# Optimization experiments

Measured on AMD Instinct MI355X. Metric: run time of the kernel, lower is better.

The kernel has to match this reference:

```python
import jax, jax.numpy as jnp
from jax import lax
import numpy as np

# ---- dims / neuron params (match init_kwargs) ----
B, T, ENC, HID = 256, 500, 700, 128
TAU_MEM = 20.0      # tauSr == tauRef == tau_mem
THETA = 1.0         # spike_threshold
SCALE_REF = 1.0
WIDTH_GRAD = 1.0    # tauRho (surrogate width)
SCALE_GRAD = 1.0    # scaleRho (surrogate scale)


def alpha_filter(x, tau, mult):
    """Causal convolution along axis 0 with SLAYER's alpha (SRM) kernel
    h[k] = mult * (k/tau) * exp(1 - k/tau), Ts = 1.  Implemented as an exact
    2-state linear recurrence instead of an O(T^2) FIR conv.
    x: (T, ...) -> y: (T, ...)
    """
    d = jnp.exp(-1.0 / tau)          # per-step decay
    c = mult * jnp.exp(1.0) / tau    # h[k] = c * k * d**k

    def step(carry, xt):
        p, q = carry
        qn = d * q + c * d * p       # output at t (h[0] = 0)
        pn = d * p + xt
        return (pn, qn), qn

    z = jnp.zeros_like(x[0])
    _, y = lax.scan(step, (z, z), x)
    return y


def _spike_core(u):
    """SLAYER getSpikes: at each t, membrane = psp + accumulated refractory
    response (alpha kernel with mult = -2*theta*scaleRef, tau = tauRef) of all
    past spikes; emit spike (1/Ts) when membrane >= theta.
    u: (T, B, C) psp values -> (spikes, post-refractory membrane), both (T, B, C).
    """
    d = jnp.exp(-1.0 / TAU_MEM)
    c = (-2.0 * THETA * SCALE_REF) * jnp.exp(1.0) / TAU_MEM

    def step(carry, ut):
        p, q = carry
        qn = d * q + c * d * p       # refractory contribution at t (0 from spike at t)
        u_t = ut + qn                # membrane after refractory subtraction
        s_t = (u_t >= THETA).astype(ut.dtype)
        pn = d * p + s_t
        return (pn, qn), (s_t, u_t)

    z = jnp.zeros_like(u[0])
    _, (s, u_post) = lax.scan(step, (z, z), u)
    return s, u_post


@jax.custom_vjp
def spike(u):
    return _spike_core(u)[0]


def _spike_fwd(u):
    s, u_post = _spike_core(u)
    return s, u_post


def _spike_bwd(u_post, g):
    # SLAYER surrogate: pdf = scaleRho / (tauRho*theta) * exp(-|u - theta| / (tauRho*theta)),
    # evaluated on the refractory-modified membrane; grad does not flow through
    # the refractory recurrence (matches the torch autograd.Function).
    tc = WIDTH_GRAD * THETA
    pdf = (SCALE_GRAD / tc) * jnp.exp(-jnp.abs(u_post - THETA) / tc)
    return (g * pdf,)


spike.defvjp(_spike_fwd, _spike_bwd)


def setup_inputs():
    key = jax.random.key(0)
    k1, k2, k3 = jax.random.split(key, 3)
    # sparse binary input spike trains (B, T, ENC)
    x = (jax.random.uniform(k1, (B, T, ENC)) < 0.05).astype(jnp.float32)
    w1 = jax.random.normal(k2, (HID, ENC), dtype=jnp.float32) * 0.1
    w2 = jax.random.normal(k3, (1, HID), dtype=jnp.float32) * 0.3
    return {"x": x, "w1": w1, "w2": w2}


def reference(x, w1, w2):
    # x: (B, T, ENC) -> time-major (T, B, ENC) for the temporal scans
    xt = jnp.transpose(x, (1, 0, 2))
    h = jnp.einsum('tbc,hc->tbh', xt, w1)        # slayer.dense (bias-free linear per step)
    h = alpha_filter(h, TAU_MEM, 1.0)            # slayer.psp
    s1 = spike(h)                                # slayer.spike (threshold + refractory)
    o = jnp.einsum('tbh,oh->tbo', s1, w2)
    o = alpha_filter(o, TAU_MEM, 1.0)
    s2 = spike(o)
    return jnp.transpose(s2, (1, 0, 2))          # (B, T, 1), matches out2.movedim(-1, 1)
```

## Files before the change

### kernel.cpp

```cpp
#include <hip/hip_runtime.h>

#define BB  256
#define TT  500
#define ENC 700
#define ENC_PAD 704
#define HID 128

__global__ __launch_bounds__(128) void transpose_w1_kernel(const float* __restrict__ w1,
                                                           float* __restrict__ w1t) {
    int c = blockIdx.x;
    int h = threadIdx.x;
    w1t[c * HID + h] = (c < ENC) ? w1[h * ENC + c] : 0.0f;
}

__global__ __launch_bounds__(256, 4) void spmm4_kernel(const float* __restrict__ x,
                                                       const float* __restrict__ w1t,
                                                       float* __restrict__ h) {
    __shared__ ushort lists[8][152];
    const int lane = threadIdx.x & 63;
    const int w = threadIdx.x >> 6;
    const int rbase = blockIdx.x * 8 + w * 2;
    const unsigned long long lt = (1ull << lane) - 1ull;

    const float* xrowA = x + (size_t)rbase * ENC;
    const float* xrowB = xrowA + ENC;
    float xva[11], xvb[11];
    #pragma unroll
    for (int k = 0; k < 11; ++k) {
        int c = k * 64 + lane;
        xva[k] = (c < ENC) ? xrowA[c] : 0.0f;
    }
    #pragma unroll
    for (int k = 0; k < 11; ++k) {
        int c = k * 64 + lane;
        xvb[k] = (c < ENC) ? xrowB[c] : 0.0f;
    }

    int nA = 0, nB = 0;
    #pragma unroll
    for (int k = 0; k < 11; ++k) {
        bool act = (xva[k] != 0.0f);
        unsigned long long m = __ballot(act);
        if (act) {
            int pos = nA + (int)__popcll(m & lt);
            if (pos < 144) lists[2 * w + 0][pos] = (ushort)(k * 64 + lane);
        }
        nA += (int)__popcll(m);
    }
    #pragma unroll
    for (int k = 0; k < 11; ++k) {
        bool act = (xvb[k] != 0.0f);
        unsigned long long m = __ballot(act);
        if (act) {
            int pos = nB + (int)__popcll(m & lt);
            if (pos < 144) lists[2 * w + 1][pos] = (ushort)(k * 64 + lane);
        }
        nB += (int)__popcll(m);
    }
    nA = (nA < 144) ? nA : 144;
    nB = (nB < 144) ? nB : 144;
    int npmax = ((nA > nB ? nA : nB) + 3) & ~3;
    if (npmax < 4) npmax = 4;
    for (int p = nA + lane; p < npmax + 4; p += 64) lists[2 * w + 0][p] = (ushort)ENC;
    for (int p = nB + lane; p < npmax + 4; p += 64) lists[2 * w + 1][p] = (ushort)ENC;

    const int half = lane >> 5;
    const int hl = lane & 31;
    const ushort* mylist = lists[2 * w + half];
    const float* wb = w1t + 4 * hl;

    float a0 = 0.f, a1 = 0.f, a2 = 0.f, a3 = 0.f;

    int c0 = mylist[0], c1 = mylist[1], c2 = mylist[2], c3 = mylist[3];
    float4 p0 = *(const float4*)(wb + (size_t)c0 * HID);
    float4 p1 = *(const float4*)(wb + (size_t)c1 * HID);
    float4 p2 = *(const float4*)(wb + (size_t)c2 * HID);
    float4 p3 = *(const float4*)(wb + (size_t)c3 * HID);

    for (int j = 0; j < npmax; j += 4) {
        int d0 = mylist[j + 4], d1 = mylist[j + 5];
        int d2 = mylist[j + 6], d3 = mylist[j + 7];
        float4 q0 = *(const float4*)(wb + (size_t)d0 * HID);
        float4 q1 = *(const float4*)(wb + (size_t)d1 * HID);
        float4 q2 = *(const float4*)(wb + (size_t)d2 * HID);
        float4 q3 = *(const float4*)(wb + (size_t)d3 * HID);
        a0 += p0.x; a1 += p0.y; a2 += p0.z; a3 += p0.w;
        a0 += p1.x; a1 += p1.y; a2 += p1.z; a3 += p1.w;
        a0 += p2.x; a1 += p2.y; a2 += p2.z; a3 += p2.w;
        a0 += p3.x; a1 += p3.y; a2 += p3.z; a3 += p3.w;
        p0 = q0; p1 = q1; p2 = q2; p3 = q3;
    }

    const int r = rbase + half;
    float4* dst = (float4*)(h + (size_t)r * HID) + hl;
    *dst = make_float4(a0, a1, a2, a3);
}

__global__ __launch_bounds__(128) void recur_kernel(const float* __restrict__ hgl,
                                                    const float* __restrict__ w2,
                                                    float* __restrict__ out) {
    __shared__ float vbuf[50 * 129];
    __shared__ float pbuf[2][50];

    const int b = blockIdx.x;
    const int tid = threadIdx.x;

    const float D   = 0.95122942450071400910f;
    const float CD  = (float)(0.13591409142295226 * 0.95122942450071400910);
    const float CRD = (float)(-0.27182818284590452 * 0.95122942450071400910);

    float ap = 0.f, aq = 0.f, rp = 0.f, rq = 0.f;
    float Ap = 0.f, Aq = 0.f, Rp = 0.f, Rq = 0.f;
    const float w2v = w2[tid];

    const float* hb = hgl + (size_t)b * (TT * HID) + tid;

    float hA[50], hB[50];

    auto body = [&](const float (&hv)[50], int chunk) {
        #pragma unroll
        for (int tl = 0; tl < 50; ++tl) {
            float h_ = hv[tl];
            float y = fmaf(D, aq, CD * ap);
            aq = y;
            ap = fmaf(D, ap, h_);
            float q = fmaf(D, rq, CRD * rp);
            float u = y + q;
            float s = (u >= 1.0f) ? 1.0f : 0.0f;
            rq = q;
            rp = fmaf(D, rp, s);
            vbuf[tl * 129 + tid] = s * w2v;
        }
        __syncthreads();

        if (tid < 50) {
            const float* row = &vbuf[tid * 129];
            float a0 = 0.f, a1 = 0.f, a2 = 0.f, a3 = 0.f;
            #pragma unroll
            for (int k = 0; k < 64; k += 4) {
                a0 += row[k]; a1 += row[k + 1]; a2 += row[k + 2]; a3 += row[k + 3];
            }
            pbuf[0][tid] = (a0 + a1) + (a2 + a3);
        } else if (tid >= 64 && tid < 114) {
            const float* row = &vbuf[(tid - 64) * 129 + 64];
            float a0 = 0.f, a1 = 0.f, a2 = 0.f, a3 = 0.f;
            #pragma unroll
            for (int k = 0; k < 64; k += 4) {
                a0 += row[k]; a1 += row[k + 1]; a2 += row[k + 2]; a3 += row[k + 3];
            }
            pbuf[1][tid - 64] = (a0 + a1) + (a2 + a3);
        }
        __syncthreads();

        float my_s2 = 0.f;
        #pragma unroll
        for (int tl = 0; tl < 50; ++tl) {
            float ot = pbuf[0][tl] + pbuf[1][tl];
            float y2 = fmaf(D, Aq, CD * Ap);
            Aq = y2;
            Ap = fmaf(D, Ap, ot);
            float q2 = fmaf(D, Rq, CRD * Rp);
            float u2 = y2 + q2;
            float s2 = (u2 >= 1.0f) ? 1.0f : 0.0f;
            Rq = q2;
            Rp = fmaf(D, Rp, s2);
            if (tl == tid) my_s2 = s2;
        }
        if (tid < 50) out[(size_t)b * TT + chunk * 50 + tid] = my_s2;
    };

    #pragma unroll
    for (int j = 0; j < 50; ++j) hA[j] = hb[j * HID];

    for (int cp = 0; cp < 5; ++cp) {
        {
            const float* g = hb + (size_t)(2 * cp + 1) * 50 * HID;
            #pragma unroll
            for (int j = 0; j < 50; ++j) hB[j] = g[j * HID];
        }
        body(hA, 2 * cp);
        if (cp < 4) {
            const float* g = hb + (size_t)(2 * cp + 2) * 50 * HID;
            #pragma unroll
            for (int j = 0; j < 50; ++j) hA[j] = g[j * HID];
        }
        body(hB, 2 * cp + 1);
    }
}

extern "C" void kernel_launch(void* const* d_in, const int* in_sizes, int n_in,
                              void* d_out, int out_size, void* d_ws, size_t ws_size,
                              hipStream_t stream) {
    const float* x  = (const float*)d_in[0];
    const float* w1 = (const float*)d_in[1];
    const float* w2 = (const float*)d_in[2];
    float* out = (float*)d_out;

    float* h   = (float*)d_ws;
    float* w1t = h + (size_t)TT * BB * HID;

    hipLaunchKernelGGL(transpose_w1_kernel, dim3(ENC_PAD), dim3(HID), 0, stream, w1, w1t);
    hipLaunchKernelGGL(spmm4_kernel, dim3((BB * TT) / 8), dim3(256), 0, stream, x, w1t, h);
    hipLaunchKernelGGL(recur_kernel, dim3(BB), dim3(128), 0, stream, h, w2, out);
}
```

Baseline: 590.4 us.

## Fuse sparse input projection into recurrence kernel with producer/consumer warps

Merges the sparse gather-matmul and the temporal recurrence into one kernel, with one block per batch element. Warps 2–3 build the next 50-step chunk of hidden inputs into a double-buffered LDS tile while warps 0–1 run the spiking recurrence on the current chunk. This removes the global write and re-read of the full hidden tensor and one kernel launch. The cost is that the projection now runs on only 256 blocks, each with two producer warps, so reading the input and gathering weights loses most of its GPU-wide parallelism and may become latency-bound.

```diff
diff --git a/kernel.cpp b/kernel.cpp
--- a/kernel.cpp
+++ b/kernel.cpp
@@ -13,123 +13,134 @@
     w1t[c * HID + h] = (c < ENC) ? w1[h * ENC + c] : 0.0f;
 }
 
-__global__ __launch_bounds__(256, 4) void spmm4_kernel(const float* __restrict__ x,
+__global__ __launch_bounds__(256, 1) void fused_kernel(const float* __restrict__ x,
                                                        const float* __restrict__ w1t,
-                                                       float* __restrict__ h) {
-    __shared__ ushort lists[8][152];
-    const int lane = threadIdx.x & 63;
-    const int w = threadIdx.x >> 6;
-    const int rbase = blockIdx.x * 8 + w * 2;
-    const unsigned long long lt = (1ull << lane) - 1ull;
-
-    const float* xrowA = x + (size_t)rbase * ENC;
-    const float* xrowB = xrowA + ENC;
-    float xva[11], xvb[11];
-    #pragma unroll
-    for (int k = 0; k < 11; ++k) {
-        int c = k * 64 + lane;
-        xva[k] = (c < ENC) ? xrowA[c] : 0.0f;
-    }
-    #pragma unroll
-    for (int k = 0; k < 11; ++k) {
-        int c = k * 64 + lane;
-        xvb[k] = (c < ENC) ? xrowB[c] : 0.0f;
-    }
-
-    int nA = 0, nB = 0;
-    #pragma unroll
-    for (int k = 0; k < 11; ++k) {
-        bool act = (xva[k] != 0.0f);
-        unsigned long long m = __ballot(act);
-        if (act) {
-            int pos = nA + (int)__popcll(m & lt);
-            if (pos < 144) lists[2 * w + 0][pos] = (ushort)(k * 64 + lane);
-        }
-        nA += (int)__popcll(m);
-    }
-    #pragma unroll
-    for (int k = 0; k < 11; ++k) {
-        bool act = (xvb[k] != 0.0f);
-        unsigned long long m = __ballot(act);
-        if (act) {
-            int pos = nB + (int)__popcll(m & lt);
-            if (pos < 144) lists[2 * w + 1][pos] = (ushort)(k * 64 + lane);
-        }
-        nB += (int)__popcll(m);
-    }
-    nA = (nA < 144) ? nA : 144;
-    nB = (nB < 144) ? nB : 144;
-    int npmax = ((nA > nB ? nA : nB) + 3) & ~3;
-    if (npmax < 4) npmax = 4;
-    for (int p = nA + lane; p < npmax + 4; p += 64) lists[2 * w + 0][p] = (ushort)ENC;
-    for (int p = nB + lane; p < npmax + 4; p += 64) lists[2 * w + 1][p] = (ushort)ENC;
-
-    const int half = lane >> 5;
-    const int hl = lane & 31;
-    const ushort* mylist = lists[2 * w + half];
-    const float* wb = w1t + 4 * hl;
-
-    float a0 = 0.f, a1 = 0.f, a2 = 0.f, a3 = 0.f;
-
-    int c0 = mylist[0], c1 = mylist[1], c2 = mylist[2], c3 = mylist[3];
-    float4 p0 = *(const float4*)(wb + (size_t)c0 * HID);
-    float4 p1 = *(const float4*)(wb + (size_t)c1 * HID);
-    float4 p2 = *(const float4*)(wb + (size_t)c2 * HID);
-    float4 p3 = *(const float4*)(wb + (size_t)c3 * HID);
-
-    for (int j = 0; j < npmax; j += 4) {
-        int d0 = mylist[j + 4], d1 = mylist[j + 5];
-        int d2 = mylist[j + 6], d3 = mylist[j + 7];
-        float4 q0 = *(const float4*)(wb + (size_t)d0 * HID);
-        float4 q1 = *(const float4*)(wb + (size_t)d1 * HID);
-        float4 q2 = *(const float4*)(wb + (size_t)d2 * HID);
-        float4 q3 = *(const float4*)(wb + (size_t)d3 * HID);
-        a0 += p0.x; a1 += p0.y; a2 += p0.z; a3 += p0.w;
-        a0 += p1.x; a1 += p1.y; a2 += p1.z; a3 += p1.w;
-        a0 += p2.x; a1 += p2.y; a2 += p2.z; a3 += p2.w;
-        a0 += p3.x; a1 += p3.y; a2 += p3.z; a3 += p3.w;
-        p0 = q0; p1 = q1; p2 = q2; p3 = q3;
-    }
-
-    const int r = rbase + half;
-    float4* dst = (float4*)(h + (size_t)r * HID) + hl;
-    *dst = make_float4(a0, a1, a2, a3);
-}
-
-__global__ __launch_bounds__(128) void recur_kernel(const float* __restrict__ hgl,
-                                                    const float* __restrict__ w2,
-                                                    float* __restrict__ out) {
+                                                       const float* __restrict__ w2,
+                                                       float* __restrict__ out) {
+    __shared__ float hb[2][50 * 128];
     __shared__ float vbuf[50 * 129];
     __shared__ float pbuf[2][50];
+    __shared__ ushort lists[8][152];
 
-    const int b = blockIdx.x;
-    const int tid = threadIdx.x;
+    const int tid  = threadIdx.x;
+    const int lane = tid & 63;
+    const int wid  = tid >> 6;
+    const int b    = blockIdx.x;
+    const unsigned long long lt = (1ull << lane) - 1ull;
 
     const float D   = 0.95122942450071400910f;
     const float CD  = (float)(0.13591409142295226 * 0.95122942450071400910);
     const float CRD = (float)(-0.27182818284590452 * 0.95122942450071400910);
 
+    auto produce_pair = [&](int buf, int chunk, int t0) {
+        const int half = lane >> 5;
+        const int hl   = lane & 31;
+        const float* xrowA = x + ((size_t)b * TT + (size_t)chunk * 50 + t0) * ENC;
+        const float* xrowB = xrowA + ENC;
+
+        float xva[11], xvb[11];
+        #pragma unroll
+        for (int k = 0; k < 11; ++k) {
+            int c = k * 64 + lane;
+            xva[k] = (c < ENC) ? xrowA[c] : 0.0f;
+        }
+        #pragma unroll
+        for (int k = 0; k < 11; ++k) {
+            int c = k * 64 + lane;
+            xvb[k] = (c < ENC) ? xrowB[c] : 0.0f;
+        }
+
+        int nA = 0, nB = 0;
+        #pragma unroll
+        for (int k = 0; k < 11; ++k) {
+            bool act = (xva[k] != 0.0f);
+            unsigned long long m = __ballot(act);
+            if (act) {
+                int pos = nA + (int)__popcll(m & lt);
+                if (pos < 144) lists[2 * wid + 0][pos] = (ushort)(k * 64 + lane);
+            }
+            nA += (int)__popcll(m);
+        }
+        #pragma unroll
+        for (int k = 0; k < 11; ++k) {
+            bool act = (xvb[k] != 0.0f);
+            unsigned long long m = __ballot(act);
+            if (act) {
+                int pos = nB + (int)__popcll(m & lt);
+                if (pos < 144) lists[2 * wid + 1][pos] = (ushort)(k * 64 + lane);
+            }
+            nB += (int)__popcll(m);
+        }
+        nA = (nA < 144) ? nA : 144;
+        nB = (nB < 144) ? nB : 144;
+        int npmax = ((nA > nB ? nA : nB) + 3) & ~3;
+        if (npmax < 4) npmax = 4;
+        for (int p = nA + lane; p < npmax + 4; p += 64) lists[2 * wid + 0][p] = (ushort)ENC;
+        for (int p = nB + lane; p < npmax + 4; p += 64) lists[2 * wid + 1][p] = (ushort)ENC;
+
+        const ushort* mylist = lists[2 * wid + half];
+        const float* wb = w1t + 4 * hl;
+
+        float a0 = 0.f, a1 = 0.f, a2 = 0.f, a3 = 0.f;
+        int c0 = mylist[0], c1 = mylist[1], c2 = mylist[2], c3 = mylist[3];
+        float4 p0 = *(const float4*)(wb + (size_t)c0 * HID);
+        float4 p1 = *(const float4*)(wb + (size_t)c1 * HID);
+        float4 p2 = *(const float4*)(wb + (size_t)c2 * HID);
+        float4 p3 = *(const float4*)(wb + (size_t)c3 * HID);
+        for (int j = 0; j < npmax; j += 4) {
+            int d0 = mylist[j + 4], d1 = mylist[j + 5];
+            int d2 = mylist[j + 6], d3 = mylist[j + 7];
+            float4 q0 = *(const float4*)(wb + (size_t)d0 * HID);
+            float4 q1 = *(const float4*)(wb + (size_t)d1 * HID);
+            float4 q2 = *(const float4*)(wb + (size_t)d2 * HID);
+            float4 q3 = *(const float4*)(wb + (size_t)d3 * HID);
+            a0 += p0.x; a1 += p0.y; a2 += p0.z; a3 += p0.w;
+            a0 += p1.x; a1 += p1.y; a2 += p1.z; a3 += p1.w;
+            a0 += p2.x; a1 += p2.y; a2 += p2.z; a3 += p2.w;
+            a0 += p3.x; a1 += p3.y; a2 += p3.z; a3 += p3.w;
+            p0 = q0; p1 = q1; p2 = q2; p3 = q3;
+        }
+        float4* dst = (float4*)&hb[buf][(t0 + half) * 128] + hl;
+        *dst = make_float4(a0, a1, a2, a3);
+    };
+
+    const float w2v = (tid < HID) ? w2[tid] : 0.0f;
+
     float ap = 0.f, aq = 0.f, rp = 0.f, rq = 0.f;
     float Ap = 0.f, Aq = 0.f, Rp = 0.f, Rq = 0.f;
-    const float w2v = w2[tid];
 
-    const float* hb = hgl + (size_t)b * (TT * HID) + tid;
+    {
+        const int base  = (wid == 0) ? 0 : (wid == 1) ? 14 : (wid == 2) ? 26 : 38;
+        const int pairs = (wid == 0) ? 7 : 6;
+        for (int it = 0; it < pairs; ++it) produce_pair(0, 0, base + 2 * it);
+    }
+    __syncthreads();
 
-    float hA[50], hB[50];
+    for (int chunk = 0; chunk < 10; ++chunk) {
+        const int cur = chunk & 1;
 
-    auto body = [&](const float (&hv)[50], int chunk) {
-        #pragma unroll
-        for (int tl = 0; tl < 50; ++tl) {
-            float h_ = hv[tl];
-            float y = fmaf(D, aq, CD * ap);
-            aq = y;
-            ap = fmaf(D, ap, h_);
-            float q = fmaf(D, rq, CRD * rp);
-            float u = y + q;
-            float s = (u >= 1.0f) ? 1.0f : 0.0f;
-            rq = q;
-            rp = fmaf(D, rp, s);
-            vbuf[tl * 129 + tid] = s * w2v;
+        if (wid >= 2) {
+            if (chunk < 9) {
+                const int base  = (wid == 2) ? 0 : 26;
+                const int pairs = (wid == 2) ? 13 : 12;
+                for (int it = 0; it < pairs; ++it)
+                    produce_pair(cur ^ 1, chunk + 1, base + 2 * it);
+            }
+        } else {
+            const float* hrow = &hb[cur][0];
+            #pragma unroll
+            for (int tl = 0; tl < 50; ++tl) {
+                float h_ = hrow[tl * 128 + tid];
+                float y = fmaf(D, aq, CD * ap);
+                aq = y;
+                ap = fmaf(D, ap, h_);
+                float q = fmaf(D, rq, CRD * rp);
+                float u = y + q;
+                float s = (u >= 1.0f) ? 1.0f : 0.0f;
+                rq = q;
+                rp = fmaf(D, rp, s);
+                vbuf[tl * 129 + tid] = s * w2v;
+            }
         }
         __syncthreads();
 
@@ -152,39 +163,23 @@
         }
         __syncthreads();
 
-        float my_s2 = 0.f;
-        #pragma unroll
-        for (int tl = 0; tl < 50; ++tl) {
-            float ot = pbuf[0][tl] + pbuf[1][tl];
-            float y2 = fmaf(D, Aq, CD * Ap);
-            Aq = y2;
-            Ap = fmaf(D, Ap, ot);
-            float q2 = fmaf(D, Rq, CRD * Rp);
-            float u2 = y2 + q2;
-            float s2 = (u2 >= 1.0f) ? 1.0f : 0.0f;
-            Rq = q2;
-            Rp = fmaf(D, Rp, s2);
-            if (tl == tid) my_s2 = s2;
+        if (tid < 128) {
+            float my_s2 = 0.f;
+            #pragma unroll
+            for (int tl = 0; tl < 50; ++tl) {
+                float ot = pbuf[0][tl] + pbuf[1][tl];
+                float y2 = fmaf(D, Aq, CD * Ap);
+                Aq = y2;
+                Ap = fmaf(D, Ap, ot);
+                float q2 = fmaf(D, Rq, CRD * Rp);
+                float u2 = y2 + q2;
+                float s2 = (u2 >= 1.0f) ? 1.0f : 0.0f;
+                Rq = q2;
+                Rp = fmaf(D, Rp, s2);
+                if (tl == tid) my_s2 = s2;
+            }
+            if (tid < 50) out[(size_t)b * TT + chunk * 50 + tid] = my_s2;
         }
-        if (tid < 50) out[(size_t)b * TT + chunk * 50 + tid] = my_s2;
-    };
-
-    #pragma unroll
-    for (int j = 0; j < 50; ++j) hA[j] = hb[j * HID];
-
-    for (int cp = 0; cp < 5; ++cp) {
-        {
-            const float* g = hb + (size_t)(2 * cp + 1) * 50 * HID;
-            #pragma unroll
-            for (int j = 0; j < 50; ++j) hB[j] = g[j * HID];
-        }
-        body(hA, 2 * cp);
-        if (cp < 4) {
-            const float* g = hb + (size_t)(2 * cp + 2) * 50 * HID;
-            #pragma unroll
-            for (int j = 0; j < 50; ++j) hA[j] = g[j * HID];
-        }
-        body(hB, 2 * cp + 1);
     }
 }
 
@@ -196,10 +191,8 @@
     const float* w2 = (const float*)d_in[2];
     float* out = (float*)d_out;
 
-    float* h   = (float*)d_ws;
-    float* w1t = h + (size_t)TT * BB * HID;
+    float* w1t = (float*)d_ws;
 
     hipLaunchKernelGGL(transpose_w1_kernel, dim3(ENC_PAD), dim3(HID), 0, stream, w1, w1t);
-    hipLaunchKernelGGL(spmm4_kernel, dim3((BB * TT) / 8), dim3(256), 0, stream, x, w1t, h);
-    hipLaunchKernelGGL(recur_kernel, dim3(BB), dim3(128), 0, stream, h, w2, out);
+    hipLaunchKernelGGL(fused_kernel, dim3(BB), dim3(256), 0, stream, x, w1t, w2, out);
 }
```

After: 952.7 us. 61.4% more time.

## Pipeline layer-2 recurrence on a dedicated extra wavefront overlapping layer-1 chunks

Applied to the files above, without the earlier changes.

Adds a third wavefront to the recurrence block that runs the serial layer-2 scan for the previous 50-step chunk while the first two wavefronts compute the layer-1 recurrence for the current chunk. The partial-sum buffer is double-buffered by chunk parity so the two stages do not overwrite each other. This takes the serial layer-2 scan off the critical path of each chunk. In exchange the block grows to 192 threads and adds a final drain step for the last chunk.

```diff
diff --git a/kernel.cpp b/kernel.cpp
--- a/kernel.cpp
+++ b/kernel.cpp
@@ -96,11 +96,11 @@
     *dst = make_float4(a0, a1, a2, a3);
 }
 
-__global__ __launch_bounds__(128) void recur_kernel(const float* __restrict__ hgl,
+__global__ __launch_bounds__(192) void recur_kernel(const float* __restrict__ hgl,
                                                     const float* __restrict__ w2,
                                                     float* __restrict__ out) {
     __shared__ float vbuf[50 * 129];
-    __shared__ float pbuf[2][50];
+    __shared__ float pbuf[2][2][50];
 
     const int b = blockIdx.x;
     const int tid = threadIdx.x;
@@ -111,51 +111,19 @@
 
     float ap = 0.f, aq = 0.f, rp = 0.f, rq = 0.f;
     float Ap = 0.f, Aq = 0.f, Rp = 0.f, Rq = 0.f;
-    const float w2v = w2[tid];
+    const float w2v = (tid < HID) ? w2[tid] : 0.0f;
 
     const float* hb = hgl + (size_t)b * (TT * HID) + tid;
 
     float hA[50], hB[50];
 
-    auto body = [&](const float (&hv)[50], int chunk) {
+    auto layer2 = [&](int chunk) {
+        const int par = chunk & 1;
+        const int t2 = tid - 128;
+        float my2 = 0.f;
         #pragma unroll
         for (int tl = 0; tl < 50; ++tl) {
-            float h_ = hv[tl];
-            float y = fmaf(D, aq, CD * ap);
-            aq = y;
-            ap = fmaf(D, ap, h_);
-            float q = fmaf(D, rq, CRD * rp);
-            float u = y + q;
-            float s = (u >= 1.0f) ? 1.0f : 0.0f;
-            rq = q;
-            rp = fmaf(D, rp, s);
-            vbuf[tl * 129 + tid] = s * w2v;
-        }
-        __syncthreads();
-
-        if (tid < 50) {
-            const float* row = &vbuf[tid * 129];
-            float a0 = 0.f, a1 = 0.f, a2 = 0.f, a3 = 0.f;
-            #pragma unroll
-            for (int k = 0; k < 64; k += 4) {
-                a0 += row[k]; a1 += row[k + 1]; a2 += row[k + 2]; a3 += row[k + 3];
-            }
-            pbuf[0][tid] = (a0 + a1) + (a2 + a3);
-        } else if (tid >= 64 && tid < 114) {
-            const float* row = &vbuf[(tid - 64) * 129 + 64];
-            float a0 = 0.f, a1 = 0.f, a2 = 0.f, a3 = 0.f;
-            #pragma unroll
-            for (int k = 0; k < 64; k += 4) {
-                a0 += row[k]; a1 += row[k + 1]; a2 += row[k + 2]; a3 += row[k + 3];
-            }
-            pbuf[1][tid - 64] = (a0 + a1) + (a2 + a3);
-        }
-        __syncthreads();
-
-        float my_s2 = 0.f;
-        #pragma unroll
-        for (int tl = 0; tl < 50; ++tl) {
-            float ot = pbuf[0][tl] + pbuf[1][tl];
+            float ot = pbuf[par][0][tl] + pbuf[par][1][tl];
             float y2 = fmaf(D, Aq, CD * Ap);
             Aq = y2;
             Ap = fmaf(D, Ap, ot);
@@ -164,28 +132,72 @@
             float s2 = (u2 >= 1.0f) ? 1.0f : 0.0f;
             Rq = q2;
             Rp = fmaf(D, Rp, s2);
-            if (tl == tid) my_s2 = s2;
-        }
-        if (tid < 50) out[(size_t)b * TT + chunk * 50 + tid] = my_s2;
+            if (tl == t2) my2 = s2;
+        }
+        if (t2 < 50) out[(size_t)b * TT + chunk * 50 + t2] = my2;
     };
 
-    #pragma unroll
-    for (int j = 0; j < 50; ++j) hA[j] = hb[j * HID];
+    auto body = [&](const float (&hv)[50], int chunk) {
+        if (tid < 128) {
+            #pragma unroll
+            for (int tl = 0; tl < 50; ++tl) {
+                float h_ = hv[tl];
+                float y = fmaf(D, aq, CD * ap);
+                aq = y;
+                ap = fmaf(D, ap, h_);
+                float q = fmaf(D, rq, CRD * rp);
+                float u = y + q;
+                float s = (u >= 1.0f) ? 1.0f : 0.0f;
+                rq = q;
+                rp = fmaf(D, rp, s);
+                vbuf[tl * 129 + tid] = s * w2v;
+            }
+        } else if (chunk >= 1) {
+            layer2(chunk - 1);
+        }
+        __syncthreads();
+
+        if (tid < 50) {
+            const float* row = &vbuf[tid * 129];
+            float a0 = 0.f, a1 = 0.f, a2 = 0.f, a3 = 0.f;
+            #pragma unroll
+            for (int k = 0; k < 64; k += 4) {
+                a0 += row[k]; a1 += row[k + 1]; a2 += row[k + 2]; a3 += row[k + 3];
+            }
+            pbuf[chunk & 1][0][tid] = (a0 + a1) + (a2 + a3);
+        } else if (tid >= 64 && tid < 114) {
+            const float* row = &vbuf[(tid - 64) * 129 + 64];
+            float a0 = 0.f, a1 = 0.f, a2 = 0.f, a3 = 0.f;
+            #pragma unroll
+            for (int k = 0; k < 64; k += 4) {
+                a0 += row[k]; a1 += row[k + 1]; a2 += row[k + 2]; a3 += row[k + 3];
+            }
+            pbuf[chunk & 1][1][tid - 64] = (a0 + a1) + (a2 + a3);
+        }
+        __syncthreads();
+    };
+
+    if (tid < 128) {
+        #pragma unroll
+        for (int j = 0; j < 50; ++j) hA[j] = hb[j * HID];
+    }
 
     for (int cp = 0; cp < 5; ++cp) {
-        {
+        if (tid < 128) {
             const float* g = hb + (size_t)(2 * cp + 1) * 50 * HID;
             #pragma unroll
             for (int j = 0; j < 50; ++j) hB[j] = g[j * HID];
         }
         body(hA, 2 * cp);
-        if (cp < 4) {
+        if (cp < 4 && tid < 128) {
             const float* g = hb + (size_t)(2 * cp + 2) * 50 * HID;
             #pragma unroll
             for (int j = 0; j < 50; ++j) hA[j] = g[j * HID];
         }
         body(hB, 2 * cp + 1);
     }
+
+    if (tid >= 128) layer2(9);
 }
 
 extern "C" void kernel_launch(void* const* d_in, const int* in_sizes, int n_in,
@@ -201,5 +213,5 @@
 
     hipLaunchKernelGGL(transpose_w1_kernel, dim3(ENC_PAD), dim3(HID), 0, stream, w1, w1t);
     hipLaunchKernelGGL(spmm4_kernel, dim3((BB * TT) / 8), dim3(256), 0, stream, x, w1t, h);
-    hipLaunchKernelGGL(recur_kernel, dim3(BB), dim3(128), 0, stream, h, w2, out);
-}
+    hipLaunchKernelGGL(recur_kernel, dim3(BB), dim3(192), 0, stream, h, w2, out);
+}
```

Measured after the change: 803.5 us. +36.1%, slower.
